# Performance work log

Hardware: AMD Instinct MI355X
Metric: run time of the kernel (lower is better)

## Reference

```python
import jax, jax.numpy as jnp
import numpy as np

N, D, H, E = 8192, 1024, 4096, 8


def setup_inputs() -> dict:
    key = jax.random.key(0)
    ks = jax.random.split(key, 5)
    s_in = 1.0 / np.sqrt(D)
    s_h = 1.0 / np.sqrt(H)
    return {
        "x": jax.random.normal(ks[0], (N, D), dtype=jnp.float32),
        "Wg": jax.random.normal(ks[1], (D, E), dtype=jnp.float32) * s_in,
        "bg": jnp.zeros((E,), dtype=jnp.float32),
        "W1": jax.random.normal(ks[2], (E, D, H), dtype=jnp.float32) * s_in,
        "b1": jnp.zeros((E, H), dtype=jnp.float32),
        "W2": jax.random.normal(ks[3], (E, H, D), dtype=jnp.float32) * s_h,
        "b2": jnp.zeros((E, D), dtype=jnp.float32),
    }


def reference(x, Wg, bg, W1, b1, W2, b2):
    # gate: softmax linear router -> weights [N, E]
    weights = jax.nn.softmax(x @ Wg + bg, axis=-1)
    # all experts, batched GEMMs: h [N, E, H]
    h = jax.nn.relu(jnp.einsum("nd,edh->neh", x, W1) + b1)  # Dropout is identity at inference
    outputs = jnp.einsum("neh,ehd->ned", h, W2) + b2         # [N, E, D]
    # weighted combine over experts
    return jnp.einsum("ne,ned->nd", weights, outputs)
```

## Files before the change

kernel.cpp:

```cpp
#include <hip/hip_runtime.h>
#include <hip/hip_bf16.h>

#define DDIM 1024
#define HDIM 4096
#define NEXP 8
#define NROW 8192
#define KPAIR 8192

typedef __attribute__((ext_vector_type(8))) short s16x8;
typedef __attribute__((ext_vector_type(4))) float f32x4;

using bf16 = __hip_bfloat16;

__device__ __forceinline__ void gload16(const bf16* g, bf16* lds) {
    __builtin_amdgcn_global_load_lds(
        (const __attribute__((address_space(1))) unsigned int*)g,
        (__attribute__((address_space(3))) unsigned int*)lds,
        16, 0, 0);
}

template <int N>
__device__ __forceinline__ void wait_vmcnt() {
    if constexpr (N == 6)      asm volatile("s_waitcnt vmcnt(6)" ::: "memory");
    else if constexpr (N == 3) asm volatile("s_waitcnt vmcnt(3)" ::: "memory");
    else                       asm volatile("s_waitcnt vmcnt(0)" ::: "memory");
}

__global__ void cvtgate_kernel(const float* __restrict__ x, const float* __restrict__ Wg,
                               const float* __restrict__ bg, bf16* __restrict__ xb,
                               float* __restrict__ wts) {
    int wave = threadIdx.x >> 6, lane = threadIdx.x & 63;
    int n = blockIdx.x * 4 + wave;
    const float* xr = x + (size_t)n * DDIM;
    bf16* xbr = xb + (size_t)n * DDIM;
    float acc[NEXP] = {0.f, 0.f, 0.f, 0.f, 0.f, 0.f, 0.f, 0.f};
#pragma unroll
    for (int j = 0; j < 4; ++j) {
        int d0 = j * 256 + lane * 4;
        float4 v = *(const float4*)&xr[d0];
        union { bf16 b[4]; uint2 u; } pk;
        pk.b[0] = __float2bfloat16(v.x);
        pk.b[1] = __float2bfloat16(v.y);
        pk.b[2] = __float2bfloat16(v.z);
        pk.b[3] = __float2bfloat16(v.w);
        *(uint2*)&xbr[d0] = pk.u;
        const float* w0 = Wg + (size_t)d0 * NEXP;
#pragma unroll
        for (int e = 0; e < NEXP; ++e)
            acc[e] += v.x * w0[e] + v.y * w0[NEXP + e] + v.z * w0[2 * NEXP + e] +
                      v.w * w0[3 * NEXP + e];
    }
#pragma unroll
    for (int off = 32; off > 0; off >>= 1) {
#pragma unroll
        for (int e = 0; e < NEXP; ++e) acc[e] += __shfl_xor(acc[e], off, 64);
    }
    if (lane == 0) {
        float mx = -1e30f;
#pragma unroll
        for (int e = 0; e < NEXP; ++e) { acc[e] += bg[e]; mx = fmaxf(mx, acc[e]); }
        float s = 0.f;
#pragma unroll
        for (int e = 0; e < NEXP; ++e) { acc[e] = __expf(acc[e] - mx); s += acc[e]; }
        float inv = 1.0f / s;
#pragma unroll
        for (int e = 0; e < NEXP; ++e) wts[(size_t)n * NEXP + e] = acc[e] * inv;
    }
}

__global__ void transpose_cvt_kernel(const float* __restrict__ src, bf16* __restrict__ dst,
                                     int R, int C, int ldo, size_t szs, int dzo) {
    __shared__ float t[128][65];
    const float* s = src + (size_t)blockIdx.z * szs;
    bf16* d = dst + (size_t)blockIdx.z * dzo;
    const int r0 = blockIdx.y * 64, c0 = blockIdx.x * 128;
    const int tid = threadIdx.x;
    const int lrow = tid >> 5, lc4 = tid & 31;
#pragma unroll
    for (int i = 0; i < 8; ++i) {
        int rr = i * 8 + lrow;
        float4 v = *(const float4*)&s[(size_t)(r0 + rr) * C + c0 + lc4 * 4];
        t[lc4 * 4 + 0][rr] = v.x;
        t[lc4 * 4 + 1][rr] = v.y;
        t[lc4 * 4 + 2][rr] = v.z;
        t[lc4 * 4 + 3][rr] = v.w;
    }
    __syncthreads();
    const int oc = tid >> 3, oj = tid & 7;
#pragma unroll
    for (int i = 0; i < 4; ++i) {
        int c = oc + i * 32;
        union { bf16 b[8]; s16x8 v; } p;
#pragma unroll
        for (int q = 0; q < 8; ++q) p.b[q] = __float2bfloat16(t[c][oj * 8 + q]);
        *(s16x8*)&d[(size_t)(c0 + c) * ldo + r0 + oj * 8] = p.v;
    }
}

__global__ void out_init_kernel(const float* __restrict__ wts, const float* __restrict__ b2,
                                float* __restrict__ out) {
    size_t idx = (size_t)blockIdx.x * 256 + threadIdx.x;
    int d = (int)(idx & (DDIM - 1));
    size_t n = idx >> 10;
    const float* w = wts + n * NEXP;
    float s = 0.f;
#pragma unroll
    for (int e = 0; e < NEXP; ++e) s += w[e] * b2[(size_t)e * DDIM + d];
    out[idx] = s;
}

__global__ __launch_bounds__(512, 1) void gemm1(
    const bf16* __restrict__ A, const bf16* __restrict__ BTp, bf16* __restrict__ Hsb,
    const float* __restrict__ b1p, const float* __restrict__ wts,
    int lda, int ldb, int ldc, int NT, int tilesM, int tilesN, int XGN, int e0) {
    constexpr int WROWS = 128;
    constexpr int HALFA = 256 * 32;
    constexpr int HALFB = 256 * 32;
    constexpr int ATOT = 2 * HALFA;
    constexpr int BUFE = ATOT + 2 * HALFB;
    __shared__ __align__(16) bf16 smem[2 * BUFE];

    const int tid = threadIdx.x;
    const int wave = tid >> 6, lane = tid & 63;
    const int wm = wave >> 2, wn = wave & 3;
    const int r = lane & 15, kg = lane >> 4;

    const int eh = blockIdx.x >> 9;
    const int bx = blockIdx.x & 511;
    const bf16* BT = BTp + (size_t)eh * HDIM * DDIM;
    bf16* Cout = Hsb + (size_t)eh * HDIM;
    const float* bias = b1p + (size_t)eh * HDIM;
    const int expert = e0 + eh;

    const int xcd = bx & 7, slot = bx >> 3;
    const int XGM = 8 / XGN;
    const int rm = tilesM / XGM, rn = tilesN / XGN;
    const int g = slot >> 5, u = slot & 31;
    const int gpr = rn >> 3;
    const int gm = (g / gpr) * 4 + (u >> 3);
    const int gn = (g % gpr) * 8 + (u & 7);
    const int tm = (xcd / XGN) * rm + gm;
    const int tn = (xcd % XGN) * rn + gn;

    const bf16* gA = A + (size_t)tm * 256 * lda;
    const bf16* gB = BT + (size_t)tn * 256 * ldb;

    f32x4 acc[8][4];
#pragma unroll
    for (int m = 0; m < 8; ++m)
#pragma unroll
        for (int n = 0; n < 4; ++n) acc[m][n] = (f32x4){0.f, 0.f, 0.f, 0.f};

    auto stageA = [&](int t, int ks) {
        bf16* dst = smem + (t & 1) * BUFE + ks * HALFA;
#pragma unroll
        for (int j = 0; j < 2; ++j) {
            int c = j * 512 + tid;
            int R = c >> 2, kc = (c & 3) ^ ((R >> 1) & 3);
            gload16(gA + (size_t)R * lda + t * 64 + ks * 32 + kc * 8,
                    dst + (j * 512 + wave * 64) * 8);
        }
    };
    auto stageB = [&](int t, int ks) {
        bf16* dst = smem + (t & 1) * BUFE + ATOT + ks * HALFB;
#pragma unroll
        for (int j = 0; j < 2; ++j) {
            int c = j * 512 + tid;
            int R = c >> 2, kc = (c & 3) ^ ((R >> 1) & 3);
            gload16(gB + (size_t)R * ldb + t * 64 + ks * 32 + kc * 8,
                    dst + (j * 512 + wave * 64) * 8);
        }
    };

    s16x8 a0[4], bb[4];
    auto ldA = [&](int buf, int ks, int mh) {
#pragma unroll
        for (int m = 0; m < 4; ++m) {
            int R = wm * WROWS + mh * 64 + m * 16 + r;
            a0[m] = *(const s16x8*)&smem[buf * BUFE + ks * HALFA + R * 32 +
                                         ((kg ^ ((R >> 1) & 3)) * 8)];
        }
    };
    auto ldB = [&](int buf, int ks) {
#pragma unroll
        for (int n = 0; n < 4; ++n) {
            int R = wn * 64 + n * 16 + r;
            bb[n] = *(const s16x8*)&smem[buf * BUFE + ATOT + ks * HALFB + R * 32 +
                                         ((kg ^ ((R >> 1) & 3)) * 8)];
        }
    };

    auto preMFMA = [&]() {
        __builtin_amdgcn_s_barrier();
        asm volatile("s_waitcnt lgkmcnt(0)" ::: "memory");
        __builtin_amdgcn_sched_barrier(0);
        __builtin_amdgcn_s_setprio(1);
    };
    auto postMFMA = [&](bool vm) {
        __builtin_amdgcn_s_setprio(0);
        if (vm) wait_vmcnt<6>();
        __builtin_amdgcn_s_barrier();
    };
    auto mfmaLo = [&]() {
#pragma unroll
        for (int m = 0; m < 4; ++m)
#pragma unroll
            for (int n = 0; n < 4; ++n)
                acc[m][n] = __builtin_amdgcn_mfma_f32_16x16x32_bf16(a0[m], bb[n], acc[m][n], 0, 0, 0);
    };
    auto mfmaHi = [&]() {
#pragma unroll
        for (int m = 0; m < 4; ++m)
#pragma unroll
            for (int n = 0; n < 4; ++n)
                acc[4 + m][n] = __builtin_amdgcn_mfma_f32_16x16x32_bf16(a0[m], bb[n], acc[4 + m][n], 0, 0, 0);
    };

    stageB(0, 0); stageA(0, 0); stageB(0, 1); stageA(0, 1);
    stageB(1, 0); stageA(1, 0); stageB(1, 1);
    wait_vmcnt<6>();
    __builtin_amdgcn_s_barrier();

    const int NI = NT / 2;
    for (int i = 0; i < NI; ++i) {
        const int t0 = 2 * i, t1 = t0 + 1;
        const bool g2 = (t0 + 2 < NT), g3 = (t1 + 2 < NT);
        ldB(0, 0); ldA(0, 0, 0); stageA(t1, 1);
        preMFMA(); mfmaLo(); postMFMA(false);
        ldA(0, 0, 1); if (g2) stageB(t0 + 2, 0);
        preMFMA(); mfmaHi(); postMFMA(false);
        ldB(0, 1); ldA(0, 1, 0); if (g2) stageA(t0 + 2, 0);
        preMFMA(); mfmaLo(); postMFMA(false);
        ldA(0, 1, 1); if (g2) stageB(t0 + 2, 1);
        preMFMA(); mfmaHi(); postMFMA(true);
        ldB(1, 0); ldA(1, 0, 0); if (g2) stageA(t0 + 2, 1);
        preMFMA(); mfmaLo(); postMFMA(false);
        ldA(1, 0, 1); if (g3) stageB(t1 + 2, 0);
        preMFMA(); mfmaHi(); postMFMA(false);
        ldB(1, 1); ldA(1, 1, 0); if (g3) stageA(t1 + 2, 0);
        preMFMA(); mfmaLo(); postMFMA(false);
        ldA(1, 1, 1); if (g3) stageB(t1 + 2, 1);
        preMFMA(); mfmaHi(); postMFMA(true);
    }

    bf16* hs = smem;
    const int col0 = tn * 256 + wn * 64;
#pragma unroll
    for (int n = 0; n < 4; ++n) {
        float bv = bias[col0 + n * 16 + r];
        int cl = wn * 64 + n * 16 + r;
#pragma unroll
        for (int mf = 0; mf < 8; ++mf) {
#pragma unroll
            for (int j = 0; j < 4; ++j) {
                int rl = wm * WROWS + (mf >> 2) * 64 + (mf & 3) * 16 + kg * 4 + j;
                float wv = wts[((size_t)tm * 256 + rl) * NEXP + expert];
                float v = acc[mf][n][j] + bv;
                v = v > 0.f ? v : 0.f;
                hs[rl * 256 + (cl ^ ((rl & 7) << 3))] = __float2bfloat16(wv * v);
            }
        }
    }
    __builtin_amdgcn_s_barrier();
    asm volatile("s_waitcnt lgkmcnt(0)" ::: "memory");
    const size_t rbase = (size_t)tm * 256;
    const int cbase = tn * 256;
#pragma unroll
    for (int i2 = 0; i2 < 16; ++i2) {
        int rl = wave * 32 + i2 * 2 + (lane >> 5);
        int c8 = (lane & 31) * 8;
        s16x8 v = *(const s16x8*)&hs[rl * 256 + (c8 ^ ((rl & 7) << 3))];
        *(s16x8*)&Cout[(rbase + rl) * (size_t)ldc + cbase + c8] = v;
    }
}

__global__ __launch_bounds__(512, 1) void gemm2pair(
    const bf16* __restrict__ A, const bf16* __restrict__ BT, float* __restrict__ O,
    int lda, int ldb, int ldc, int NT, int tilesM, int tilesN, int XGN) {
    constexpr int HALFA = 256 * 32;
    constexpr int HALFB = 128 * 32;
    constexpr int ATOT = 2 * HALFA;
    constexpr int BUFE = ATOT + 2 * HALFB;
    constexpr int RSTR = 68;
    __shared__ __align__(16) bf16 smem[3 * BUFE];

    const int tid = threadIdx.x;
    const int wave = tid >> 6, lane = tid & 63;
    const int ksw = wave & 1, wn = (wave >> 1) & 1, wm = wave >> 2;
    const int r = lane & 15, kg = lane >> 4;

    const int xcd = blockIdx.x & 7, slot = blockIdx.x >> 3;
    const int XGM = 8 / XGN;
    const int rm = tilesM / XGM, rn = tilesN / XGN;
    const int g = slot >> 5, u = slot & 31;
    const int gpr = rn >> 3;
    const int gm = (g / gpr) * 4 + (u >> 3);
    const int gn = (g % gpr) * 8 + (u & 7);
    const int tm = (xcd / XGN) * rm + gm;
    const int tn = (xcd % XGN) * rn + gn;

    const bf16* gA = A + (size_t)tm * 256 * lda;
    const bf16* gB = BT + (size_t)tn * 128 * ldb;

    f32x4 acc[8][4];
#pragma unroll
    for (int m = 0; m < 8; ++m)
#pragma unroll
        for (int n = 0; n < 4; ++n) acc[m][n] = (f32x4){0.f, 0.f, 0.f, 0.f};

    auto stageA = [&](int t, int ks) {
        bf16* dst = smem + (t % 3) * BUFE + ks * HALFA;
#pragma unroll
        for (int j = 0; j < 2; ++j) {
            int c = j * 512 + tid;
            int R = c >> 2, kc = (c & 3) ^ ((R >> 1) & 3);
            gload16(gA + (size_t)R * lda + t * 64 + ks * 32 + kc * 8,
                    dst + (j * 512 + wave * 64) * 8);
        }
    };
    auto stageB = [&](int t, int ks) {
        bf16* dst = smem + (t % 3) * BUFE + ATOT + ks * HALFB;
        int R = tid >> 2, kc = (tid & 3) ^ ((R >> 1) & 3);
        gload16(gB + (size_t)R * ldb + t * 64 + ks * 32 + kc * 8, dst + (wave * 64) * 8);
    };

    s16x8 a0[4], a1[4], bfr[4];
    auto ldA0 = [&](int rb) {
#pragma unroll
        for (int m = 0; m < 4; ++m) {
            int R = wm * 128 + m * 16 + r;
            a0[m] = *(const s16x8*)&smem[rb * BUFE + ksw * HALFA + R * 32 +
                                         ((kg ^ ((R >> 1) & 3)) * 8)];
        }
    };
    auto ldA1 = [&](int rb) {
#pragma unroll
        for (int m = 0; m < 4; ++m) {
            int R = wm * 128 + 64 + m * 16 + r;
            a1[m] = *(const s16x8*)&smem[rb * BUFE + ksw * HALFA + R * 32 +
                                         ((kg ^ ((R >> 1) & 3)) * 8)];
        }
    };
    auto ldB = [&](int rb) {
#pragma unroll
        for (int n = 0; n < 4; ++n) {
            int R = wn * 64 + n * 16 + r;
            bfr[n] = *(const s16x8*)&smem[rb * BUFE + ATOT + ksw * HALFB + R * 32 +
                                          ((kg ^ ((R >> 1) & 3)) * 8)];
        }
    };

    stageA(0, 0); stageB(0, 0); stageA(0, 1); stageB(0, 1);
    stageA(1, 0); stageB(1, 0); stageA(1, 1); stageB(1, 1);
    wait_vmcnt<6>();
    __builtin_amdgcn_s_barrier();

    for (int t = 0; t < NT; ++t) {
        const int rb = t % 3;
        const bool gg = (t + 2 < NT);
        ldB(rb); ldA0(rb);
        if (gg) { stageA(t + 2, 0); stageB(t + 2, 0); }
        ldA1(rb);
        if (gg) { stageA(t + 2, 1); stageB(t + 2, 1); }
        asm volatile("s_waitcnt lgkmcnt(4)" ::: "memory");
        __builtin_amdgcn_sched_barrier(0);
        __builtin_amdgcn_s_setprio(1);
#pragma unroll
        for (int m = 0; m < 4; ++m)
#pragma unroll
            for (int n = 0; n < 4; ++n)
                acc[m][n] = __builtin_amdgcn_mfma_f32_16x16x32_bf16(a0[m], bfr[n], acc[m][n], 0, 0, 0);
        __builtin_amdgcn_s_setprio(0);
        asm volatile("s_waitcnt lgkmcnt(0)" ::: "memory");
        __builtin_amdgcn_sched_barrier(0);
        __builtin_amdgcn_s_setprio(1);
#pragma unroll
        for (int m = 0; m < 4; ++m)
#pragma unroll
            for (int n = 0; n < 4; ++n)
                acc[4 + m][n] = __builtin_amdgcn_mfma_f32_16x16x32_bf16(a1[m], bfr[n], acc[4 + m][n], 0, 0, 0);
        __builtin_amdgcn_s_setprio(0);
        if (t + 1 < NT) {
            if (gg) wait_vmcnt<6>();
            else    wait_vmcnt<0>();
            __builtin_amdgcn_s_barrier();
        }
    }

    __syncthreads();
    float* red = (float*)smem;
    const int zb0 = ((wm * 2 + wn) * 2 + 0) * (64 * RSTR);
    const int zb1 = ((wm * 2 + wn) * 2 + 1) * (64 * RSTR);
    if (ksw == 1) {
#pragma unroll
        for (int mq = 0; mq < 4; ++mq) {
#pragma unroll
            for (int n = 0; n < 4; ++n) {
                int rl = mq * 16 + kg * 4;
                int cl = n * 16 + r;
#pragma unroll
                for (int j = 0; j < 4; ++j)
                    red[zb0 + (rl + j) * RSTR + cl] = acc[mq][n][j];
            }
        }
    } else {
#pragma unroll
        for (int mq = 0; mq < 4; ++mq) {
#pragma unroll
            for (int n = 0; n < 4; ++n) {
                int rl = mq * 16 + kg * 4;
                int cl = n * 16 + r;
#pragma unroll
                for (int j = 0; j < 4; ++j)
                    red[zb1 + (rl + j) * RSTR + cl] = acc[4 + mq][n][j];
            }
        }
    }
    __syncthreads();
    const int col0 = tn * 128 + wn * 64;
    if (ksw == 0) {
        const size_t row0 = (size_t)tm * 256 + wm * 128;
#pragma unroll
        for (int mq = 0; mq < 4; ++mq) {
#pragma unroll
            for (int j = 0; j < 4; ++j) {
                int rl = mq * 16 + kg * 4 + j;
                size_t rr = row0 + rl;
#pragma unroll
                for (int n = 0; n < 4; ++n) {
                    int cl = n * 16 + r;
                    float v = acc[mq][n][j] + red[zb0 + rl * RSTR + cl];
                    O[rr * (size_t)ldc + col0 + cl] += v;
                }
            }
        }
    } else {
        const size_t row0 = (size_t)tm * 256 + wm * 128 + 64;
#pragma unroll
        for (int mq = 0; mq < 4; ++mq) {
#pragma unroll
            for (int j = 0; j < 4; ++j) {
                int rl = mq * 16 + kg * 4 + j;
                size_t rr = row0 + rl;
#pragma unroll
                for (int n = 0; n < 4; ++n) {
                    int cl = n * 16 + r;
                    float v = acc[4 + mq][n][j] + red[zb1 + rl * RSTR + cl];
                    O[rr * (size_t)ldc + col0 + cl] += v;
                }
            }
        }
    }
}

extern "C" void kernel_launch(void* const* d_in, const int* in_sizes, int n_in,
                              void* d_out, int out_size, void* d_ws, size_t ws_size,
                              hipStream_t stream) {
    const float* x  = (const float*)d_in[0];
    const float* Wg = (const float*)d_in[1];
    const float* bg = (const float*)d_in[2];
    const float* W1 = (const float*)d_in[3];
    const float* b1 = (const float*)d_in[4];
    const float* W2 = (const float*)d_in[5];
    const float* b2 = (const float*)d_in[6];
    float* out = (float*)d_out;

    char* ws = (char*)d_ws;
    bf16* xb   = (bf16*)(ws);
    bf16* W1P  = (bf16*)(ws + (16ull << 20));
    bf16* W2P  = (bf16*)(ws + (32ull << 20));
    bf16* Hs   = (bf16*)(ws + (48ull << 20));
    float* wts = (float*)(ws + (176ull << 20));

    cvtgate_kernel<<<NROW / 4, 256, 0, stream>>>(x, Wg, bg, xb, wts);
    out_init_kernel<<<NROW * DDIM / 256, 256, 0, stream>>>(wts, b2, out);

    for (int p = 0; p < 4; ++p) {
        transpose_cvt_kernel<<<dim3(HDIM / 128, DDIM / 64, 2), 256, 0, stream>>>(
            W1 + (size_t)2 * p * DDIM * HDIM, W1P, DDIM, HDIM, DDIM,
            (size_t)DDIM * HDIM, HDIM * DDIM);
        gemm1<<<1024, 512, 0, stream>>>(
            xb, W1P, Hs, b1 + (size_t)2 * p * HDIM, wts,
            DDIM, DDIM, KPAIR, DDIM / 64, 32, 16, 2, 2 * p);
        transpose_cvt_kernel<<<dim3(DDIM / 128, HDIM / 64, 2), 256, 0, stream>>>(
            W2 + (size_t)2 * p * HDIM * DDIM, W2P, HDIM, DDIM, KPAIR,
            (size_t)HDIM * DDIM, HDIM);
        gemm2pair<<<256, 512, 0, stream>>>(
            Hs, W2P, out, KPAIR, KPAIR, DDIM, KPAIR / 64, 32, 8, 1);
    }
}
```

Before: 1.277 ms.

## Restructure gemm2 into 128x128 tiles with 4 waves and two blocks per CU

```diff
diff --git a/kernel.cpp b/kernel.cpp
--- a/kernel.cpp
+++ b/kernel.cpp
@@ -274,19 +274,19 @@
     }
 }
 
-__global__ __launch_bounds__(512, 1) void gemm2pair(
+__global__ __launch_bounds__(256, 2) void gemm2p(
     const bf16* __restrict__ A, const bf16* __restrict__ BT, float* __restrict__ O,
     int lda, int ldb, int ldc, int NT, int tilesM, int tilesN, int XGN) {
-    constexpr int HALFA = 256 * 32;
+    constexpr int HALFA = 128 * 32;
     constexpr int HALFB = 128 * 32;
     constexpr int ATOT = 2 * HALFA;
     constexpr int BUFE = ATOT + 2 * HALFB;
     constexpr int RSTR = 68;
-    __shared__ __align__(16) bf16 smem[3 * BUFE];
+    __shared__ __align__(16) bf16 smem[2 * BUFE];
 
     const int tid = threadIdx.x;
     const int wave = tid >> 6, lane = tid & 63;
-    const int ksw = wave & 1, wn = (wave >> 1) & 1, wm = wave >> 2;
+    const int ksw = wave & 1, wn = wave >> 1;
     const int r = lane & 15, kg = lane >> 4;
 
     const int xcd = blockIdx.x & 7, slot = blockIdx.x >> 3;
@@ -299,7 +299,7 @@
     const int tm = (xcd / XGN) * rm + gm;
     const int tn = (xcd % XGN) * rn + gn;
 
-    const bf16* gA = A + (size_t)tm * 256 * lda;
+    const bf16* gA = A + (size_t)tm * 128 * lda;
     const bf16* gB = BT + (size_t)tn * 128 * ldb;
 
     f32x4 acc[8][4];
@@ -308,148 +308,148 @@
 #pragma unroll
         for (int n = 0; n < 4; ++n) acc[m][n] = (f32x4){0.f, 0.f, 0.f, 0.f};
 
-    auto stageA = [&](int t, int ks) {
-        bf16* dst = smem + (t % 3) * BUFE + ks * HALFA;
+    auto stageA_rh = [&](int t, int rh) {
+        bf16* base = smem + (t & 1) * BUFE;
 #pragma unroll
         for (int j = 0; j < 2; ++j) {
-            int c = j * 512 + tid;
-            int R = c >> 2, kc = (c & 3) ^ ((R >> 1) & 3);
-            gload16(gA + (size_t)R * lda + t * 64 + ks * 32 + kc * 8,
-                    dst + (j * 512 + wave * 64) * 8);
-        }
-    };
-    auto stageB = [&](int t, int ks) {
-        bf16* dst = smem + (t % 3) * BUFE + ATOT + ks * HALFB;
-        int R = tid >> 2, kc = (tid & 3) ^ ((R >> 1) & 3);
-        gload16(gB + (size_t)R * ldb + t * 64 + ks * 32 + kc * 8, dst + (wave * 64) * 8);
-    };
-
-    s16x8 a0[4], a1[4], bfr[4];
-    auto ldA0 = [&](int rb) {
+            int c = j * 256 + tid;
+            int Rl = (c >> 2) & 63;
+            int R = rh * 64 + Rl;
+            int kc = (c & 3) ^ ((R >> 1) & 3);
+            gload16(gA + (size_t)R * lda + t * 64 + j * 32 + kc * 8,
+                    base + j * HALFA + rh * 2048 + ((c & 255) - lane) * 8 + lane * 8);
+        }
+    };
+    auto stageB = [&](int t) {
+        bf16* base = smem + (t & 1) * BUFE + ATOT;
+#pragma unroll
+        for (int j = 0; j < 4; ++j) {
+            int c = j * 256 + tid;
+            int ks = c >> 9;
+            int R = (c >> 2) & 127;
+            int kc = (c & 3) ^ ((R >> 1) & 3);
+            gload16(gB + (size_t)R * ldb + t * 64 + ks * 32 + kc * 8,
+                    base + ks * HALFB + ((c & 511) - lane) * 8 + lane * 8);
+        }
+    };
+
+    s16x8 afr[4], bfr[4];
+    auto ldA = [&](int b, int mh) {
 #pragma unroll
         for (int m = 0; m < 4; ++m) {
-            int R = wm * 128 + m * 16 + r;
-            a0[m] = *(const s16x8*)&smem[rb * BUFE + ksw * HALFA + R * 32 +
-                                         ((kg ^ ((R >> 1) & 3)) * 8)];
-        }
-    };
-    auto ldA1 = [&](int rb) {
-#pragma unroll
-        for (int m = 0; m < 4; ++m) {
-            int R = wm * 128 + 64 + m * 16 + r;
-            a1[m] = *(const s16x8*)&smem[rb * BUFE + ksw * HALFA + R * 32 +
-                                         ((kg ^ ((R >> 1) & 3)) * 8)];
-        }
-    };
-    auto ldB = [&](int rb) {
+            int R = mh * 64 + m * 16 + r;
+            afr[m] = *(const s16x8*)&smem[b * BUFE + ksw * HALFA + R * 32 +
+                                          ((kg ^ ((R >> 1) & 3)) * 8)];
+        }
+    };
+    auto ldB = [&](int b) {
 #pragma unroll
         for (int n = 0; n < 4; ++n) {
             int R = wn * 64 + n * 16 + r;
-            bfr[n] = *(const s16x8*)&smem[rb * BUFE + ATOT + ksw * HALFB + R * 32 +
+            bfr[n] = *(const s16x8*)&smem[b * BUFE + ATOT + ksw * HALFB + R * 32 +
                                           ((kg ^ ((R >> 1) & 3)) * 8)];
         }
     };
 
-    stageA(0, 0); stageB(0, 0); stageA(0, 1); stageB(0, 1);
-    stageA(1, 0); stageB(1, 0); stageA(1, 1); stageB(1, 1);
-    wait_vmcnt<6>();
-    __builtin_amdgcn_s_barrier();
-
-    for (int t = 0; t < NT; ++t) {
-        const int rb = t % 3;
-        const bool gg = (t + 2 < NT);
-        ldB(rb); ldA0(rb);
-        if (gg) { stageA(t + 2, 0); stageB(t + 2, 0); }
-        ldA1(rb);
-        if (gg) { stageA(t + 2, 1); stageB(t + 2, 1); }
-        asm volatile("s_waitcnt lgkmcnt(4)" ::: "memory");
-        __builtin_amdgcn_sched_barrier(0);
-        __builtin_amdgcn_s_setprio(1);
-#pragma unroll
-        for (int m = 0; m < 4; ++m)
-#pragma unroll
-            for (int n = 0; n < 4; ++n)
-                acc[m][n] = __builtin_amdgcn_mfma_f32_16x16x32_bf16(a0[m], bfr[n], acc[m][n], 0, 0, 0);
-        __builtin_amdgcn_s_setprio(0);
+    auto preMFMA = [&]() {
+        __builtin_amdgcn_s_barrier();
         asm volatile("s_waitcnt lgkmcnt(0)" ::: "memory");
         __builtin_amdgcn_sched_barrier(0);
         __builtin_amdgcn_s_setprio(1);
+    };
+
+    stageA_rh(0, 0); stageA_rh(0, 1); stageB(0);
+    stageA_rh(1, 1); stageB(1);
+    wait_vmcnt<6>();
+    __builtin_amdgcn_s_barrier();
+
+    for (int t = 0; t < NT; ++t) {
+        const int b = t & 1;
+        ldB(b); ldA(b, 1);
+        if (t + 1 < NT) stageA_rh(t + 1, 0);
+        preMFMA();
 #pragma unroll
         for (int m = 0; m < 4; ++m)
 #pragma unroll
             for (int n = 0; n < 4; ++n)
-                acc[4 + m][n] = __builtin_amdgcn_mfma_f32_16x16x32_bf16(a1[m], bfr[n], acc[4 + m][n], 0, 0, 0);
+                acc[4 + m][n] = __builtin_amdgcn_mfma_f32_16x16x32_bf16(afr[m], bfr[n], acc[4 + m][n], 0, 0, 0);
+        __builtin_amdgcn_s_setprio(0);
+        __builtin_amdgcn_s_barrier();
+        ldA(b, 0);
+        if (t + 2 < NT) { stageA_rh(t + 2, 1); stageB(t + 2); }
+        preMFMA();
+#pragma unroll
+        for (int m = 0; m < 4; ++m)
+#pragma unroll
+            for (int n = 0; n < 4; ++n)
+                acc[m][n] = __builtin_amdgcn_mfma_f32_16x16x32_bf16(afr[m], bfr[n], acc[m][n], 0, 0, 0);
         __builtin_amdgcn_s_setprio(0);
         if (t + 1 < NT) {
-            if (gg) wait_vmcnt<6>();
-            else    wait_vmcnt<0>();
+            if (t + 2 < NT) wait_vmcnt<6>();
+            else            wait_vmcnt<0>();
             __builtin_amdgcn_s_barrier();
         }
     }
 
     __syncthreads();
     float* red = (float*)smem;
-    const int zb0 = ((wm * 2 + wn) * 2 + 0) * (64 * RSTR);
-    const int zb1 = ((wm * 2 + wn) * 2 + 1) * (64 * RSTR);
+    const int zone = wn * (64 * RSTR);
+    const int col0 = tn * 128 + wn * 64;
+    const size_t row0 = (size_t)tm * 128;
     if (ksw == 1) {
 #pragma unroll
-        for (int mq = 0; mq < 4; ++mq) {
+        for (int mq = 0; mq < 4; ++mq)
 #pragma unroll
             for (int n = 0; n < 4; ++n) {
                 int rl = mq * 16 + kg * 4;
                 int cl = n * 16 + r;
 #pragma unroll
                 for (int j = 0; j < 4; ++j)
-                    red[zb0 + (rl + j) * RSTR + cl] = acc[mq][n][j];
+                    red[zone + (rl + j) * RSTR + cl] = acc[mq][n][j];
             }
-        }
-    } else {
-#pragma unroll
-        for (int mq = 0; mq < 4; ++mq) {
+    }
+    __syncthreads();
+    if (ksw == 0) {
+#pragma unroll
+        for (int mq = 0; mq < 4; ++mq)
+#pragma unroll
+            for (int j = 0; j < 4; ++j) {
+                int rl = mq * 16 + kg * 4 + j;
+                size_t rr = row0 + rl;
+#pragma unroll
+                for (int n = 0; n < 4; ++n) {
+                    int cl = n * 16 + r;
+                    O[rr * (size_t)ldc + col0 + cl] += acc[mq][n][j] + red[zone + rl * RSTR + cl];
+                }
+            }
+    }
+    __syncthreads();
+    if (ksw == 0) {
+#pragma unroll
+        for (int mq = 0; mq < 4; ++mq)
 #pragma unroll
             for (int n = 0; n < 4; ++n) {
                 int rl = mq * 16 + kg * 4;
                 int cl = n * 16 + r;
 #pragma unroll
                 for (int j = 0; j < 4; ++j)
-                    red[zb1 + (rl + j) * RSTR + cl] = acc[4 + mq][n][j];
+                    red[zone + (rl + j) * RSTR + cl] = acc[4 + mq][n][j];
             }
-        }
     }
     __syncthreads();
-    const int col0 = tn * 128 + wn * 64;
-    if (ksw == 0) {
-        const size_t row0 = (size_t)tm * 256 + wm * 128;
-#pragma unroll
-        for (int mq = 0; mq < 4; ++mq) {
+    if (ksw == 1) {
+#pragma unroll
+        for (int mq = 0; mq < 4; ++mq)
 #pragma unroll
             for (int j = 0; j < 4; ++j) {
                 int rl = mq * 16 + kg * 4 + j;
-                size_t rr = row0 + rl;
+                size_t rr = row0 + 64 + rl;
 #pragma unroll
                 for (int n = 0; n < 4; ++n) {
                     int cl = n * 16 + r;
-                    float v = acc[mq][n][j] + red[zb0 + rl * RSTR + cl];
-                    O[rr * (size_t)ldc + col0 + cl] += v;
+                    O[rr * (size_t)ldc + col0 + cl] += acc[4 + mq][n][j] + red[zone + rl * RSTR + cl];
                 }
             }
-        }
-    } else {
-        const size_t row0 = (size_t)tm * 256 + wm * 128 + 64;
-#pragma unroll
-        for (int mq = 0; mq < 4; ++mq) {
-#pragma unroll
-            for (int j = 0; j < 4; ++j) {
-                int rl = mq * 16 + kg * 4 + j;
-                size_t rr = row0 + rl;
-#pragma unroll
-                for (int n = 0; n < 4; ++n) {
-                    int cl = n * 16 + r;
-                    float v = acc[4 + mq][n][j] + red[zb1 + rl * RSTR + cl];
-                    O[rr * (size_t)ldc + col0 + cl] += v;
-                }
-            }
-        }
     }
 }
 
@@ -485,7 +485,7 @@
         transpose_cvt_kernel<<<dim3(DDIM / 128, HDIM / 64, 2), 256, 0, stream>>>(
             W2 + (size_t)2 * p * HDIM * DDIM, W2P, HDIM, DDIM, KPAIR,
             (size_t)HDIM * DDIM, HDIM);
-        gemm2pair<<<256, 512, 0, stream>>>(
-            Hs, W2P, out, KPAIR, KPAIR, DDIM, KPAIR / 64, 32, 8, 1);
-    }
-}
+        gemm2p<<<512, 256, 0, stream>>>(
+            Hs, W2P, out, KPAIR, KPAIR, DDIM, KPAIR / 64, 64, 8, 1);
+    }
+}
```

Measured after the change: 1.262 ms. About the same (-1.1%).
